# Kernel tuning notes

Measured on AMD Instinct MI355X. Metric: run time of the kernel, lower is better.

## Reference

```python
import jax, jax.numpy as jnp
import numpy as np

N_NODES = 50000
HIDDEN = 64
N_EDGES = 1200000


def setup_inputs() -> dict:
    key = jax.random.key(0)
    ks = jax.random.split(key, 12)
    x = jax.random.normal(ks[0], (N_NODES, HIDDEN), dtype=jnp.float32)
    edge_index = jax.random.randint(ks[1], (2, N_EDGES), 0, N_NODES, dtype=jnp.int64)
    s = 1.0 / np.sqrt(HIDDEN)
    # RGCN layer (single relation): relation weight, root weight, bias
    W_rel1 = jax.random.normal(ks[2], (HIDDEN, HIDDEN), dtype=jnp.float32) * s
    W_root1 = jax.random.normal(ks[3], (HIDDEN, HIDDEN), dtype=jnp.float32) * s
    b1 = jnp.zeros((HIDDEN,), dtype=jnp.float32)
    # Three GraphConv layers: self weight, neighbor weight, bias each
    W_self2 = jax.random.normal(ks[4], (HIDDEN, HIDDEN), dtype=jnp.float32) * s
    W_nbr2 = jax.random.normal(ks[5], (HIDDEN, HIDDEN), dtype=jnp.float32) * s
    b2 = jnp.zeros((HIDDEN,), dtype=jnp.float32)
    W_self3 = jax.random.normal(ks[6], (HIDDEN, HIDDEN), dtype=jnp.float32) * s
    W_nbr3 = jax.random.normal(ks[7], (HIDDEN, HIDDEN), dtype=jnp.float32) * s
    b3 = jnp.zeros((HIDDEN,), dtype=jnp.float32)
    W_self4 = jax.random.normal(ks[8], (HIDDEN, HIDDEN), dtype=jnp.float32) * s
    W_nbr4 = jax.random.normal(ks[9], (HIDDEN, HIDDEN), dtype=jnp.float32) * s
    b4 = jnp.zeros((HIDDEN,), dtype=jnp.float32)
    return {
        "x": x, "edge_index": edge_index,
        "W_rel1": W_rel1, "W_root1": W_root1, "b1": b1,
        "W_self2": W_self2, "W_nbr2": W_nbr2, "b2": b2,
        "W_self3": W_self3, "W_nbr3": W_nbr3, "b3": b3,
        "W_self4": W_self4, "W_nbr4": W_nbr4, "b4": b4,
    }


def _rgcn(x, W_rel, W_root, b, src, dst, n_nodes):
    # single-relation RGCN: root transform + mean-aggregated relation transform
    msg = x[src] @ W_rel                                   # [E, H]
    agg = jax.ops.segment_sum(msg, dst, num_segments=n_nodes)
    cnt = jax.ops.segment_sum(jnp.ones((src.shape[0],), x.dtype), dst, num_segments=n_nodes)
    agg = agg / jnp.maximum(cnt, 1.0)[:, None]
    return x @ W_root + agg + b


def _graphconv(x, W_self, W_nbr, b, src, dst, n_nodes):
    # GraphConv: self transform + sum-aggregated neighbor transform
    agg = jax.ops.segment_sum(x[src], dst, num_segments=n_nodes)  # [N, H]
    return x @ W_self + agg @ W_nbr + b


def reference(x, edge_index, W_rel1, W_root1, b1, W_self2, W_nbr2, b2,
              W_self3, W_nbr3, b3, W_self4, W_nbr4, b4):
    n = x.shape[0]
    src, dst = edge_index[0], edge_index[1]
    h = jax.nn.relu(_rgcn(x, W_rel1, W_root1, b1, src, dst, n))
    h = jax.nn.relu(_graphconv(h, W_self2, W_nbr2, b2, src, dst, n))
    x_1 = h
    h = jax.nn.relu(_graphconv(h, W_self3, W_nbr3, b3, src, dst, n))
    h = jax.nn.relu(_graphconv(h, W_self4, W_nbr4, b4, src, dst, n))
    x_2 = h
    return (x_1, x_2)
```

## Files before the change

kernel.cpp:

```cpp
#include <hip/hip_runtime.h>

#define N_NODES 50000
#define HIDDEN  64
#define N_EDGES 1200000

#define BSHIFT 7
#define BUKSZ  128
#define NBUK   391
#define GBIN   256
#define PAD2   4096

__device__ __forceinline__ float bcastf(float v, int k) {
    return __int_as_float(__builtin_amdgcn_readlane(__float_as_int(v), k));
}

__device__ __forceinline__ unsigned short f2bf(float x) {
    unsigned u = __float_as_uint(x);
    u += 0x7fffu + ((u >> 16) & 1u);
    return (unsigned short)(u >> 16);
}

__device__ __forceinline__ float bfl(unsigned w) { return __uint_as_float(w << 16); }
__device__ __forceinline__ float bfh(unsigned w) { return __uint_as_float(w & 0xffff0000u); }


__global__ __launch_bounds__(512) void init_kernel(int* __restrict__ cursor) {
    int tid = threadIdx.x;
    if (tid < NBUK) cursor[tid] = tid * PAD2;
}

__global__ __launch_bounds__(256) void scatter_fused_kernel(const int* __restrict__ ei,
                                                            int* __restrict__ cursor,
                                                            int* __restrict__ tmp, int E) {
    __shared__ int h[NBUK];
    __shared__ int cur[NBUK];
    int tid = threadIdx.x;
    for (int b = tid; b < NBUK; b += 256) h[b] = 0;
    __syncthreads();
    for (int e = blockIdx.x * 256 + tid; e < E; e += GBIN * 256)
        atomicAdd(&h[ei[E + e] >> BSHIFT], 1);
    __syncthreads();
    for (int b = tid; b < NBUK; b += 256) cur[b] = atomicAdd(&cursor[b], h[b]);
    __syncthreads();
    for (int e = blockIdx.x * 256 + tid; e < E; e += GBIN * 256) {
        int src = ei[e];
        int dst = ei[E + e];
        int p = atomicAdd(&cur[dst >> BSHIFT], 1);
        tmp[p] = src | ((dst & (BUKSZ - 1)) << 16);
    }
}

__global__ __launch_bounds__(512) void bucketize_kernel(const int* __restrict__ tmp,
                                                        const int* __restrict__ cursor,
                                                        int2* __restrict__ row_info,
                                                        unsigned short* __restrict__ csr,
                                                        int n) {
    __shared__ int hist[BUKSZ];
    __shared__ int cur[BUKSZ];
    __shared__ unsigned short stage[PAD2];
    int b = blockIdx.x, tid = threadIdx.x;
    int base = b * PAD2;
    int count = cursor[b] - base;
    int node_base = b << BSHIFT;

    if (tid < BUKSZ) hist[tid] = 0;
    __syncthreads();
    for (int i = tid; i < count; i += 512)
        atomicAdd(&hist[tmp[base + i] >> 16], 1);
    __syncthreads();
    int v = (tid < BUKSZ) ? hist[tid] : 0;
#pragma unroll
    for (int o = 1; o < BUKSZ; o <<= 1) {
        __syncthreads();
        int y = (tid >= o && tid < BUKSZ) ? hist[tid - o] : 0;
        __syncthreads();
        if (tid < BUKSZ) hist[tid] += y;
    }
    __syncthreads();
    if (tid < BUKSZ) {
        int excl = hist[tid] - v;
        cur[tid] = excl;
        int node = node_base + tid;
        if (node < n) row_info[node] = make_int2(base + excl, v);
    }
    __syncthreads();
    for (int i = tid; i < count; i += 512) {
        int p = tmp[base + i];
        int slot = atomicAdd(&cur[p >> 16], 1);
        stage[slot] = (unsigned short)(p & 0xFFFF);
    }
    __syncthreads();
    for (int i = tid; i < count; i += 512)
        csr[base + i] = stage[i];
}

__global__ __launch_bounds__(256) void gemm2_kernel(const float* __restrict__ h,
                                                    const float* __restrict__ Wnbr,
                                                    const float* __restrict__ Wself,
                                                    const float* __restrict__ bias,
                                                    unsigned short* __restrict__ tbf,
                                                    float* __restrict__ u, int n) {
    int lane = threadIdx.x & 63;
    float wn[64], ws[64];
#pragma unroll
    for (int k = 0; k < 64; ++k) {
        wn[k] = Wnbr[k * 64 + lane];
        ws[k] = Wself[k * 64 + lane];
    }
    float bv = bias[lane];
    int wave = (blockIdx.x * 256 + threadIdx.x) >> 6;
    int nwaves = gridDim.x * 4;
    if (wave == 0) tbf[(size_t)n * 64 + lane] = 0;
    for (int i = wave; i < n; i += nwaves) {
        float hv = h[i * 64 + lane];
        float tacc = 0.f, uacc = bv;
#pragma unroll
        for (int k = 0; k < 64; ++k) {
            float hk = bcastf(hv, k);
            tacc = fmaf(hk, wn[k], tacc);
            uacc = fmaf(hk, ws[k], uacc);
        }
        tbf[(size_t)i * 64 + lane] = f2bf(tacc);
        u[(size_t)i * 64 + lane] = uacc;
    }
}

__global__ __launch_bounds__(256) void agg_kernel(const unsigned short* __restrict__ tbf,
                                                  const float* __restrict__ u,
                                                  const int2* __restrict__ row_info,
                                                  const unsigned short* __restrict__ csr,
                                                  float* __restrict__ out, int n, int use_mean) {
    int lane = threadIdx.x & 63;
    int g = lane >> 4;
    int q = lane & 15;
    int node = (blockIdx.x * 256 + threadIdx.x) >> 6;
    if (node >= n) return;
    int2 ri = row_info[node];
    int start = ri.x, deg = ri.y;
    float4 a0 = {0,0,0,0}, a1 = {0,0,0,0}, a2 = {0,0,0,0}, a3 = {0,0,0,0};
    float4 a4 = {0,0,0,0}, a5 = {0,0,0,0}, a6 = {0,0,0,0}, a7 = {0,0,0,0};
    for (int e = 0; e < deg; e += 64) {
        int cnt = deg - e;
        if (cnt > 64) cnt = 64;
        int idx = (lane < cnt) ? (int)csr[start + e + lane] : n;
        int cnt32 = (cnt + 31) & ~31;
        for (int j = 0; j < cnt32; j += 32) {
            int s0 = __shfl(idx, j + g);
            int s1 = __shfl(idx, j + 4 + g);
            int s2 = __shfl(idx, j + 8 + g);
            int s3 = __shfl(idx, j + 12 + g);
            int s4 = __shfl(idx, j + 16 + g);
            int s5 = __shfl(idx, j + 20 + g);
            int s6 = __shfl(idx, j + 24 + g);
            int s7 = __shfl(idx, j + 28 + g);
            const uint2 w0 = *(const uint2*)(tbf + (size_t)s0 * 64 + q * 4);
            const uint2 w1 = *(const uint2*)(tbf + (size_t)s1 * 64 + q * 4);
            const uint2 w2 = *(const uint2*)(tbf + (size_t)s2 * 64 + q * 4);
            const uint2 w3 = *(const uint2*)(tbf + (size_t)s3 * 64 + q * 4);
            const uint2 w4 = *(const uint2*)(tbf + (size_t)s4 * 64 + q * 4);
            const uint2 w5 = *(const uint2*)(tbf + (size_t)s5 * 64 + q * 4);
            const uint2 w6 = *(const uint2*)(tbf + (size_t)s6 * 64 + q * 4);
            const uint2 w7 = *(const uint2*)(tbf + (size_t)s7 * 64 + q * 4);
            a0.x += bfl(w0.x); a0.y += bfh(w0.x); a0.z += bfl(w0.y); a0.w += bfh(w0.y);
            a1.x += bfl(w1.x); a1.y += bfh(w1.x); a1.z += bfl(w1.y); a1.w += bfh(w1.y);
            a2.x += bfl(w2.x); a2.y += bfh(w2.x); a2.z += bfl(w2.y); a2.w += bfh(w2.y);
            a3.x += bfl(w3.x); a3.y += bfh(w3.x); a3.z += bfl(w3.y); a3.w += bfh(w3.y);
            a4.x += bfl(w4.x); a4.y += bfh(w4.x); a4.z += bfl(w4.y); a4.w += bfh(w4.y);
            a5.x += bfl(w5.x); a5.y += bfh(w5.x); a5.z += bfl(w5.y); a5.w += bfh(w5.y);
            a6.x += bfl(w6.x); a6.y += bfh(w6.x); a6.z += bfl(w6.y); a6.w += bfh(w6.y);
            a7.x += bfl(w7.x); a7.y += bfh(w7.x); a7.z += bfl(w7.y); a7.w += bfh(w7.y);
        }
    }
    float4 acc;
    acc.x = ((a0.x + a1.x) + (a2.x + a3.x)) + ((a4.x + a5.x) + (a6.x + a7.x));
    acc.y = ((a0.y + a1.y) + (a2.y + a3.y)) + ((a4.y + a5.y) + (a6.y + a7.y));
    acc.z = ((a0.z + a1.z) + (a2.z + a3.z)) + ((a4.z + a5.z) + (a6.z + a7.z));
    acc.w = ((a0.w + a1.w) + (a2.w + a3.w)) + ((a4.w + a5.w) + (a6.w + a7.w));
    acc.x += __shfl_xor(acc.x, 16); acc.y += __shfl_xor(acc.y, 16);
    acc.z += __shfl_xor(acc.z, 16); acc.w += __shfl_xor(acc.w, 16);
    acc.x += __shfl_xor(acc.x, 32); acc.y += __shfl_xor(acc.y, 32);
    acc.z += __shfl_xor(acc.z, 32); acc.w += __shfl_xor(acc.w, 32);

    float scale = 1.f;
    if (use_mean) scale = 1.f / fmaxf((float)deg, 1.f);
    if (g == 0) {
        const float4 uv = *(const float4*)(u + (size_t)node * 64 + q * 4);
        float4 r;
        r.x = fmaxf(uv.x + acc.x * scale, 0.f);
        r.y = fmaxf(uv.y + acc.y * scale, 0.f);
        r.z = fmaxf(uv.z + acc.z * scale, 0.f);
        r.w = fmaxf(uv.w + acc.w * scale, 0.f);
        *(float4*)(out + (size_t)node * 64 + q * 4) = r;
    }
}


extern "C" void kernel_launch(void* const* d_in, const int* in_sizes, int n_in,
                              void* d_out, int out_size, void* d_ws, size_t ws_size,
                              hipStream_t stream) {
    const float* x      = (const float*)d_in[0];
    const int*   ei     = (const int*)d_in[1];
    const float* Wrel1  = (const float*)d_in[2];
    const float* Wroot1 = (const float*)d_in[3];
    const float* b1     = (const float*)d_in[4];
    const float* Wself2 = (const float*)d_in[5];
    const float* Wnbr2  = (const float*)d_in[6];
    const float* b2     = (const float*)d_in[7];
    const float* Wself3 = (const float*)d_in[8];
    const float* Wnbr3  = (const float*)d_in[9];
    const float* b3     = (const float*)d_in[10];
    const float* Wself4 = (const float*)d_in[11];
    const float* Wnbr4  = (const float*)d_in[12];
    const float* b4     = (const float*)d_in[13];

    const int N = N_NODES, E = N_EDGES;

    auto align = [](size_t o) { return (o + 255) & ~(size_t)255; };
    char* base = (char*)d_ws;
    size_t off = 0;
    int*  cursor   = (int*)(base + off);  off = align(off + (size_t)NBUK * 4);
    int2* row_info = (int2*)(base + off); off = align(off + (size_t)N_NODES * 8);
    int*  tmp      = (int*)(base + off);  off = align(off + (size_t)NBUK * PAD2 * 4);
    unsigned short* csr = (unsigned short*)(base + off); off = align(off + (size_t)NBUK * PAD2 * 2);
    unsigned short* tbf = (unsigned short*)(base + off); off = align(off + (size_t)(N + 1) * 64 * 2);
    float* u  = (float*)(base + off); off = align(off + (size_t)N * 64 * 4);
    float* h1 = (float*)(base + off); off = align(off + (size_t)N * 64 * 4);

    float* out1 = (float*)d_out;
    float* out2 = (float*)d_out + (size_t)N * 64;

    init_kernel<<<1, 512, 0, stream>>>(cursor);
    scatter_fused_kernel<<<GBIN, 256, 0, stream>>>(ei, cursor, tmp, E);
    bucketize_kernel<<<NBUK, 512, 0, stream>>>(tmp, cursor, row_info, csr, N);

    const int GB = 768;
    const int AB = (N + 3) / 4;

    gemm2_kernel<<<GB, 256, 0, stream>>>(x, Wrel1, Wroot1, b1, tbf, u, N);
    agg_kernel<<<AB, 256, 0, stream>>>(tbf, u, row_info, csr, h1, N, 1);
    gemm2_kernel<<<GB, 256, 0, stream>>>(h1, Wnbr2, Wself2, b2, tbf, u, N);
    agg_kernel<<<AB, 256, 0, stream>>>(tbf, u, row_info, csr, out1, N, 0);
    gemm2_kernel<<<GB, 256, 0, stream>>>(out1, Wnbr3, Wself3, b3, tbf, u, N);
    agg_kernel<<<AB, 256, 0, stream>>>(tbf, u, row_info, csr, h1, N, 0);
    gemm2_kernel<<<GB, 256, 0, stream>>>(h1, Wnbr4, Wself4, b4, tbf, u, N);
    agg_kernel<<<AB, 256, 0, stream>>>(tbf, u, row_info, csr, out2, N, 0);
}
```

Baseline: 336.1 us.

## Pad CSR rows to multiples of four and load neighbor indices as vectors

Bucketize now rounds each node's edge count up to a multiple of four when computing row offsets, so every CSR row starts 8-byte aligned. The aggregation kernel then has each 16-lane group read four neighbor indices with a single uint2 load, replacing the shuffle-based index broadcast over 64-edge chunks, and it keeps four accumulators instead of eight. The kernel also asks for 8 waves per SIMD occupancy. This is meant to cut shuffle overhead and wasted slots on low-degree nodes (around 24 edges on average), at the cost of less memory-level parallelism per wave. It also relies on padded slots being masked, which means reads may run past the actual row end.

```diff
diff --git a/kernel.cpp b/kernel.cpp
--- a/kernel.cpp
+++ b/kernel.cpp
@@ -13,13 +13,11 @@
 __device__ __forceinline__ float bcastf(float v, int k) {
     return __int_as_float(__builtin_amdgcn_readlane(__float_as_int(v), k));
 }
-
 __device__ __forceinline__ unsigned short f2bf(float x) {
     unsigned u = __float_as_uint(x);
     u += 0x7fffu + ((u >> 16) & 1u);
     return (unsigned short)(u >> 16);
 }
-
 __device__ __forceinline__ float bfl(unsigned w) { return __uint_as_float(w << 16); }
 __device__ __forceinline__ float bfh(unsigned w) { return __uint_as_float(w & 0xffff0000u); }
 
@@ -69,6 +67,9 @@
         atomicAdd(&hist[tmp[base + i] >> 16], 1);
     __syncthreads();
     int v = (tid < BUKSZ) ? hist[tid] : 0;
+    int vr = (v + 3) & ~3;
+    __syncthreads();
+    if (tid < BUKSZ) hist[tid] = vr;
 #pragma unroll
     for (int o = 1; o < BUKSZ; o <<= 1) {
         __syncthreads();
@@ -78,7 +79,7 @@
     }
     __syncthreads();
     if (tid < BUKSZ) {
-        int excl = hist[tid] - v;
+        int excl = hist[tid] - vr;
         cur[tid] = excl;
         int node = node_base + tid;
         if (node < n) row_info[node] = make_int2(base + excl, v);
@@ -90,7 +91,8 @@
         stage[slot] = (unsigned short)(p & 0xFFFF);
     }
     __syncthreads();
-    for (int i = tid; i < count; i += 512)
+    int total = hist[BUKSZ - 1];
+    for (int i = tid; i < total; i += 512)
         csr[base + i] = stage[i];
 }
 
@@ -125,11 +127,11 @@
     }
 }
 
-__global__ __launch_bounds__(256) void agg_kernel(const unsigned short* __restrict__ tbf,
-                                                  const float* __restrict__ u,
-                                                  const int2* __restrict__ row_info,
-                                                  const unsigned short* __restrict__ csr,
-                                                  float* __restrict__ out, int n, int use_mean) {
+__global__ __launch_bounds__(256, 8) void agg_kernel(const unsigned short* __restrict__ tbf,
+                                                     const float* __restrict__ u,
+                                                     const int2* __restrict__ row_info,
+                                                     const unsigned short* __restrict__ csr,
+                                                     float* __restrict__ out, int n, int use_mean) {
     int lane = threadIdx.x & 63;
     int g = lane >> 4;
     int q = lane & 15;
@@ -137,52 +139,35 @@
     if (node >= n) return;
     int2 ri = row_info[node];
     int start = ri.x, deg = ri.y;
-    float4 a0 = {0,0,0,0}, a1 = {0,0,0,0}, a2 = {0,0,0,0}, a3 = {0,0,0,0};
-    float4 a4 = {0,0,0,0}, a5 = {0,0,0,0}, a6 = {0,0,0,0}, a7 = {0,0,0,0};
-    for (int e = 0; e < deg; e += 64) {
-        int cnt = deg - e;
-        if (cnt > 64) cnt = 64;
-        int idx = (lane < cnt) ? (int)csr[start + e + lane] : n;
-        int cnt32 = (cnt + 31) & ~31;
-        for (int j = 0; j < cnt32; j += 32) {
-            int s0 = __shfl(idx, j + g);
-            int s1 = __shfl(idx, j + 4 + g);
-            int s2 = __shfl(idx, j + 8 + g);
-            int s3 = __shfl(idx, j + 12 + g);
-            int s4 = __shfl(idx, j + 16 + g);
-            int s5 = __shfl(idx, j + 20 + g);
-            int s6 = __shfl(idx, j + 24 + g);
-            int s7 = __shfl(idx, j + 28 + g);
-            const uint2 w0 = *(const uint2*)(tbf + (size_t)s0 * 64 + q * 4);
-            const uint2 w1 = *(const uint2*)(tbf + (size_t)s1 * 64 + q * 4);
-            const uint2 w2 = *(const uint2*)(tbf + (size_t)s2 * 64 + q * 4);
-            const uint2 w3 = *(const uint2*)(tbf + (size_t)s3 * 64 + q * 4);
-            const uint2 w4 = *(const uint2*)(tbf + (size_t)s4 * 64 + q * 4);
-            const uint2 w5 = *(const uint2*)(tbf + (size_t)s5 * 64 + q * 4);
-            const uint2 w6 = *(const uint2*)(tbf + (size_t)s6 * 64 + q * 4);
-            const uint2 w7 = *(const uint2*)(tbf + (size_t)s7 * 64 + q * 4);
-            a0.x += bfl(w0.x); a0.y += bfh(w0.x); a0.z += bfl(w0.y); a0.w += bfh(w0.y);
-            a1.x += bfl(w1.x); a1.y += bfh(w1.x); a1.z += bfl(w1.y); a1.w += bfh(w1.y);
-            a2.x += bfl(w2.x); a2.y += bfh(w2.x); a2.z += bfl(w2.y); a2.w += bfh(w2.y);
-            a3.x += bfl(w3.x); a3.y += bfh(w3.x); a3.z += bfl(w3.y); a3.w += bfh(w3.y);
-            a4.x += bfl(w4.x); a4.y += bfh(w4.x); a4.z += bfl(w4.y); a4.w += bfh(w4.y);
-            a5.x += bfl(w5.x); a5.y += bfh(w5.x); a5.z += bfl(w5.y); a5.w += bfh(w5.y);
-            a6.x += bfl(w6.x); a6.y += bfh(w6.x); a6.z += bfl(w6.y); a6.w += bfh(w6.y);
-            a7.x += bfl(w7.x); a7.y += bfh(w7.x); a7.z += bfl(w7.y); a7.w += bfh(w7.y);
-        }
+    const unsigned short* cp = csr + start;
+    float4 a0{0,0,0,0}, a1{0,0,0,0}, a2{0,0,0,0}, a3{0,0,0,0};
+    for (int base = 0; base < deg; base += 16) {
+        int m = base + 4 * g;
+        const uint2 iv = *(const uint2*)(cp + m);
+        int s0 = (m + 0 < deg) ? (int)(iv.x & 0xFFFF) : n;
+        int s1 = (m + 1 < deg) ? (int)(iv.x >> 16)    : n;
+        int s2 = (m + 2 < deg) ? (int)(iv.y & 0xFFFF) : n;
+        int s3 = (m + 3 < deg) ? (int)(iv.y >> 16)    : n;
+        const uint2 w0 = *(const uint2*)(tbf + (size_t)s0 * 64 + q * 4);
+        const uint2 w1 = *(const uint2*)(tbf + (size_t)s1 * 64 + q * 4);
+        const uint2 w2 = *(const uint2*)(tbf + (size_t)s2 * 64 + q * 4);
+        const uint2 w3 = *(const uint2*)(tbf + (size_t)s3 * 64 + q * 4);
+        a0.x += bfl(w0.x); a0.y += bfh(w0.x); a0.z += bfl(w0.y); a0.w += bfh(w0.y);
+        a1.x += bfl(w1.x); a1.y += bfh(w1.x); a1.z += bfl(w1.y); a1.w += bfh(w1.y);
+        a2.x += bfl(w2.x); a2.y += bfh(w2.x); a2.z += bfl(w2.y); a2.w += bfh(w2.y);
+        a3.x += bfl(w3.x); a3.y += bfh(w3.x); a3.z += bfl(w3.y); a3.w += bfh(w3.y);
     }
     float4 acc;
-    acc.x = ((a0.x + a1.x) + (a2.x + a3.x)) + ((a4.x + a5.x) + (a6.x + a7.x));
-    acc.y = ((a0.y + a1.y) + (a2.y + a3.y)) + ((a4.y + a5.y) + (a6.y + a7.y));
-    acc.z = ((a0.z + a1.z) + (a2.z + a3.z)) + ((a4.z + a5.z) + (a6.z + a7.z));
-    acc.w = ((a0.w + a1.w) + (a2.w + a3.w)) + ((a4.w + a5.w) + (a6.w + a7.w));
+    acc.x = (a0.x + a1.x) + (a2.x + a3.x);
+    acc.y = (a0.y + a1.y) + (a2.y + a3.y);
+    acc.z = (a0.z + a1.z) + (a2.z + a3.z);
+    acc.w = (a0.w + a1.w) + (a2.w + a3.w);
     acc.x += __shfl_xor(acc.x, 16); acc.y += __shfl_xor(acc.y, 16);
     acc.z += __shfl_xor(acc.z, 16); acc.w += __shfl_xor(acc.w, 16);
     acc.x += __shfl_xor(acc.x, 32); acc.y += __shfl_xor(acc.y, 32);
     acc.z += __shfl_xor(acc.z, 32); acc.w += __shfl_xor(acc.w, 32);
 
-    float scale = 1.f;
-    if (use_mean) scale = 1.f / fmaxf((float)deg, 1.f);
+    float scale = use_mean ? 1.f / fmaxf((float)deg, 1.f) : 1.f;
     if (g == 0) {
         const float4 uv = *(const float4*)(u + (size_t)node * 64 + q * 4);
         float4 r;
@@ -219,9 +204,9 @@
     char* base = (char*)d_ws;
     size_t off = 0;
     int*  cursor   = (int*)(base + off);  off = align(off + (size_t)NBUK * 4);
-    int2* row_info = (int2*)(base + off); off = align(off + (size_t)N_NODES * 8);
+    int2* row_info = (int2*)(base + off); off = align(off + (size_t)N * 8);
     int*  tmp      = (int*)(base + off);  off = align(off + (size_t)NBUK * PAD2 * 4);
-    unsigned short* csr = (unsigned short*)(base + off); off = align(off + (size_t)NBUK * PAD2 * 2);
+    unsigned short* csr = (unsigned short*)(base + off); off = align(off + (size_t)NBUK * PAD2 * 2 + 256);
     unsigned short* tbf = (unsigned short*)(base + off); off = align(off + (size_t)(N + 1) * 64 * 2);
     float* u  = (float*)(base + off); off = align(off + (size_t)N * 64 * 4);
     float* h1 = (float*)(base + off); off = align(off + (size_t)N * 64 * 4);
```

New measurement: 325.4 us. -3.2%, faster.
